# Optimization experiments

Measured on AMD Instinct MI355X. Metric: run time of the kernel, lower is better.

The kernel has to match this reference:

```python
import jax, jax.numpy as jnp
import numpy as np

NUM_HEADS = 12
LN_EPS = 1e-5
SM_EPS = 1e-6


def layer_norm(x, w, b):
    m = x.mean(-1, keepdims=True)
    v = ((x - m) ** 2).mean(-1, keepdims=True)
    return (x - m) / jnp.sqrt(v + LN_EPS) * w + b


def softmax_with_policy(attn, policy):
    # attn: [B,H,N,N], policy: [B,N,1]
    B, H, N, _ = attn.shape
    attn_policy = policy.reshape(B, 1, 1, N)
    eye = jnp.eye(N, dtype=attn.dtype)[None, None]
    attn_policy = attn_policy + (1.0 - attn_policy) * eye
    m = attn.max(axis=-1, keepdims=True)
    e = jnp.exp(attn - m) * attn_policy
    return (e + SM_EPS / N) / (e.sum(axis=-1, keepdims=True) + SM_EPS)


def create_ys(ncdf, n_ref):
    # ncdf: [B, N-1]; returns ys: [B, n_ref-1]
    B = ncdf.shape[0]
    ys = jnp.linspace(0.0, 1.0, n_ref - 1, dtype=ncdf.dtype)[None, :]
    ys_start = jnp.min(ncdf + (ncdf == 0).astype(ncdf.dtype) * 1e8, axis=1, keepdims=True)
    steps = jnp.arange(n_ref - 1, dtype=ncdf.dtype)[None, :]
    return ys_start + (ys * (n_ref - 2) - ys_start * steps) / (n_ref - 2)


def get_unique_indices(indices, max_value):
    # duplicate indices are replaced by max_value, then re-sorted
    B = indices.shape[0]
    s = jnp.sort(indices, axis=1)
    shifted = jnp.concatenate([s[:, 1:], jnp.ones((B, 1), s.dtype)], axis=1)
    uniq = jnp.where(shifted == s, max_value, s)
    return jnp.sort(uniq, axis=1)


def ats_block(x, policy, norm1_w, norm1_b, qkv_w, proj_w, proj_b,
              norm2_w, norm2_b, fc1_w, fc1_b, fc2_w, fc2_b,
              n_tokens, n_ref_tokens):
    B, N, C = x.shape
    H = NUM_HEADS
    dh = C // H
    scale = dh ** -0.5

    xn = layer_norm(x, norm1_w, norm1_b)
    qkv = (xn @ qkv_w).reshape(B, N, 3, H, dh).transpose(2, 0, 3, 1, 4)  # [3,B,H,N,dh]
    qkv = qkv * policy[None, :, None, :, :]
    q, k, v = qkv[0], qkv[1], qkv[2]

    attn = softmax_with_policy(jnp.einsum('bhnd,bhmd->bhnm', q, k) * scale, policy)

    # --- score assignment ---
    v_norm = jnp.linalg.norm(v.transpose(0, 2, 1, 3).reshape(B, N, C), axis=2)  # [B,N]
    sig = attn[:, :, 0, :].sum(axis=1) * v_norm      # CLS attention row summed over heads
    sig = sig[:, 1:]
    sig = sig / sig.sum(axis=1, keepdims=True)
    order = jnp.argsort(sig, axis=1)                 # ascending
    sorted_scores = jnp.take_along_axis(sig, order, axis=1)

    # --- inverse transform sampling ---
    cdf = jnp.cumsum(sorted_scores, axis=1)
    cmin = cdf.min(axis=1, keepdims=True)
    cmax = cdf.max(axis=1, keepdims=True)
    ncdf = (cdf - cmin) / (cmax - cmin)              # [B, N-1]
    ys = create_ys(ncdf, n_ref_tokens)               # [B, n_ref-1]
    diff = (n_ref_tokens - 1) - (N - 1)
    ncdf_p = jnp.pad(ncdf, ((0, 0), (diff, 0))) if diff > 0 else ncdf
    tokens_to_pick = jnp.argmin(jnp.abs(ys[:, :, None] - ncdf_p[:, None, :]), axis=2) - diff

    uniq = get_unique_indices(tokens_to_pick, N - 1)[:, :N - 1]
    ui = uniq[:, :n_tokens - 1]                      # [B, n_tokens-1]

    # reorder attn rows / raw tokens by significance order, pad a zero row at N-1
    oidx = jnp.broadcast_to(order[:, None, :, None], (B, H, N - 1, N))
    attn_sorted = jnp.take_along_axis(attn[:, :, 1:, :], oidx, axis=2)
    attn_tmp = jnp.pad(attn_sorted, ((0, 0), (0, 0), (0, 1), (0, 0)))
    rx_sorted = jnp.take_along_axis(x[:, 1:, :], jnp.broadcast_to(order[:, :, None], (B, N - 1, C)), axis=1)
    rx_tmp = jnp.pad(rx_sorted, ((0, 0), (0, 1), (0, 0)))

    uidx = jnp.broadcast_to(ui[:, None, :, None], (B, H, n_tokens - 1, N))
    attn_sel = jnp.take_along_axis(attn_tmp, uidx, axis=2)
    rx_sel = jnp.take_along_axis(rx_tmp, jnp.broadcast_to(ui[:, :, None], (B, n_tokens - 1, C)), axis=1)

    attn_new = jnp.concatenate([attn[:, :, 0:1, :], attn_sel], axis=2)     # [B,H,n_tokens,N]
    selected_x = jnp.concatenate([x[:, 0:1, :], rx_sel], axis=1)           # [B,n_tokens,C]
    pol_new = (ui != N - 1).astype(x.dtype)[:, :, None]
    pol_new = jnp.pad(pol_new, ((0, 0), (1, 0), (0, 0)), constant_values=1.0)  # [B,n_tokens,1]

    out = jnp.einsum('bhnm,bhmd->bhnd', attn_new, v)
    out = out.transpose(0, 2, 1, 3).reshape(B, n_tokens, C)
    out = (out @ proj_w + proj_b) * pol_new

    x2 = selected_x + out
    h = jax.nn.gelu(layer_norm(x2, norm2_w, norm2_b) @ fc1_w + fc1_b, approximate=False)
    x2 = x2 + (h @ fc2_w + fc2_b) * pol_new
    return x2, pol_new


def setup_inputs() -> dict:
    key = jax.random.key(0)
    ks = jax.random.split(key, 6)
    B, N, C = 8, 785, 768
    init = lambda k, sh, fan: jax.random.normal(k, sh, jnp.float32) * (fan ** -0.5)
    return {
        'x': jax.random.normal(ks[0], (B, N, C), jnp.float32),
        'policy': jnp.ones((B, N, 1), jnp.float32),
        'norm1_w': jnp.ones((C,), jnp.float32),
        'norm1_b': jnp.zeros((C,), jnp.float32),
        'qkv_w': init(ks[1], (C, 3 * C), C),
        'proj_w': init(ks[2], (C, C), C),
        'proj_b': jnp.zeros((C,), jnp.float32),
        'norm2_w': jnp.ones((C,), jnp.float32),
        'norm2_b': jnp.zeros((C,), jnp.float32),
        'fc1_w': init(ks[3], (C, 4 * C), C),
        'fc1_b': jnp.zeros((4 * C,), jnp.float32),
        'fc2_w': init(ks[4], (4 * C, C), 4 * C),
        'fc2_b': jnp.zeros((C,), jnp.float32),
        'n_tokens': 393,
        'n_ref_tokens': 785,
    }


def reference(x, policy, norm1_w, norm1_b, qkv_w, proj_w, proj_b,
              norm2_w, norm2_b, fc1_w, fc1_b, fc2_w, fc2_b,
              n_tokens, n_ref_tokens):
    return ats_block(x, policy, norm1_w, norm1_b, qkv_w, proj_w, proj_b,
                     norm2_w, norm2_b, fc1_w, fc1_b, fc2_w, fc2_b,
                     int(n_tokens), int(n_ref_tokens))
```

## Files before the change

kernel.cpp:

```cpp
#include <hip/hip_runtime.h>
#include <hip/hip_bf16.h>
#include <float.h>
#include <math.h>
#include <stdint.h>

constexpr int B_   = 8;
constexpr int N_   = 785;
constexpr int C_   = 768;
constexpr int H_   = 12;
constexpr int DH_  = 64;
constexpr int NT_  = 393;
constexpr int QKVC = 3 * C_;
constexpr int BN   = B_ * N_;
constexpr int BT   = B_ * NT_;
constexpr int MSEL = N_ - 1;
constexpr float  SCALE_F = 0.125f;
constexpr double LNEPS   = 1e-5;
constexpr double SMEPS   = 1e-6;

#define DEV static __device__ __forceinline__

typedef __hip_bfloat16 bf16;
typedef __attribute__((ext_vector_type(8))) short frag8;
typedef __attribute__((ext_vector_type(4))) float facc4;

DEV short f2b(float v) { return (short)__hip_bfloat16_raw(__float2bfloat16(v)).x; }
DEV float b2f(short s) {
  union { unsigned int u; float f; } cv;
  cv.u = ((unsigned int)(unsigned short)s) << 16;
  return cv.f;
}
DEV float gelu_exact(float v) { return 0.5f * v * (1.0f + erff(v * 0.70710678118654752f)); }

DEV double blockReduceSumD(double v, double* scratch, int nw) {
#pragma unroll
  for (int o = 32; o; o >>= 1) v += __shfl_xor(v, o);
  int lane = threadIdx.x & 63, wid = threadIdx.x >> 6;
  __syncthreads();
  if (lane == 0) scratch[wid] = v;
  __syncthreads();
  double r = scratch[0];
  for (int i = 1; i < nw; i++) r += scratch[i];
  return r;
}
DEV double blockReduceMaxD(double v, double* scratch, int nw) {
#pragma unroll
  for (int o = 32; o; o >>= 1) v = fmax(v, __shfl_xor(v, o));
  int lane = threadIdx.x & 63, wid = threadIdx.x >> 6;
  __syncthreads();
  if (lane == 0) scratch[wid] = v;
  __syncthreads();
  double r = scratch[0];
  for (int i = 1; i < nw; i++) r = fmax(r, scratch[i]);
  return r;
}
DEV float blockReduceSumF(float v, float* scratch, int nw) {
#pragma unroll
  for (int o = 32; o; o >>= 1) v += __shfl_xor(v, o);
  int lane = threadIdx.x & 63, wid = threadIdx.x >> 6;
  __syncthreads();
  if (lane == 0) scratch[wid] = v;
  __syncthreads();
  float r = scratch[0];
  for (int i = 1; i < nw; i++) r += scratch[i];
  return r;
}
DEV float blockReduceMaxF(float v, float* scratch, int nw) {
#pragma unroll
  for (int o = 32; o; o >>= 1) v = fmaxf(v, __shfl_xor(v, o));
  int lane = threadIdx.x & 63, wid = threadIdx.x >> 6;
  __syncthreads();
  if (lane == 0) scratch[wid] = v;
  __syncthreads();
  float r = scratch[0];
  for (int i = 1; i < nw; i++) r = fmaxf(r, scratch[i]);
  return r;
}

__global__ __launch_bounds__(256) void ln1_kernel(
    const float* __restrict__ x, const float* __restrict__ w, const float* __restrict__ b,
    double* __restrict__ xn64, bf16* __restrict__ xnb) {
  int row = blockIdx.x;
  int t = threadIdx.x;
  __shared__ double scr[8];
  const float* xr = x + (size_t)row * C_;
  double vals[3];
#pragma unroll
  for (int i = 0; i < 3; i++) vals[i] = (double)xr[t + i * 256];
  double s = vals[0] + vals[1] + vals[2];
  s = blockReduceSumD(s, scr, 4);
  double mean = s / (double)C_;
  double vs = 0.0;
#pragma unroll
  for (int i = 0; i < 3; i++) { double d = vals[i] - mean; vs += d * d; }
  vs = blockReduceSumD(vs, scr, 4);
  double inv = 1.0 / sqrt(vs / (double)C_ + LNEPS);
#pragma unroll
  for (int i = 0; i < 3; i++) {
    int c = t + i * 256;
    double o = (vals[i] - mean) * inv * (double)w[c] + (double)b[c];
    xn64[(size_t)row * C_ + c] = o;
    xnb[(size_t)row * C_ + c] = __float2bfloat16((float)o);
  }
}

__global__ __launch_bounds__(256) void transpose_bf16(
    const float* __restrict__ W, bf16* __restrict__ Wt, int K, int N) {
  __shared__ float tile[32][33];
  int k0 = blockIdx.y * 32, n0 = blockIdx.x * 32;
  int tx = threadIdx.x & 31, ty = threadIdx.x >> 5;
  for (int i = ty; i < 32; i += 8) {
    int k = k0 + i, n = n0 + tx;
    tile[i][tx] = (k < K && n < N) ? W[(size_t)k * N + n] : 0.f;
  }
  __syncthreads();
  for (int i = ty; i < 32; i += 8) {
    int n = n0 + i, k = k0 + tx;
    if (n < N && k < K) Wt[(size_t)n * K + k] = __float2bfloat16(tile[tx][i]);
  }
}

__global__ __launch_bounds__(256) void gemm128(
    const bf16* __restrict__ A, const bf16* __restrict__ Bt,
    float* __restrict__ Cc, const float* __restrict__ bias,
    const float* __restrict__ rowscale, int M, int K, int Ncols,
    bf16* __restrict__ gelu_bf) {
  __shared__ short As[128][40];
  __shared__ short Bs[128][40];
  const short* Ap = (const short*)A;
  const short* Bp = (const short*)Bt;
  int t = threadIdx.x;
  int n0 = blockIdx.x * 128;
  int m0 = blockIdx.y * 128;
  int w = t >> 6, l = t & 63;
  int wr = w >> 1, wc = w & 1;
  int srow = t >> 1;
  int koff = (t & 1) * 16;
  int fr = l & 15, fk = (l >> 4) * 8;
  facc4 acc[4][4] = {};
  for (int k0 = 0; k0 < K; k0 += 32) {
    int4 av0 = make_int4(0, 0, 0, 0), av1 = make_int4(0, 0, 0, 0);
    if (m0 + srow < M) {
      const short* ap = Ap + (size_t)(m0 + srow) * K + k0 + koff;
      av0 = *(const int4*)ap;
      av1 = *(const int4*)(ap + 8);
    }
    const short* bp = Bp + (size_t)(n0 + srow) * K + k0 + koff;
    int4 bv0 = *(const int4*)bp;
    int4 bv1 = *(const int4*)(bp + 8);
    *(int4*)(&As[srow][koff])     = av0;
    *(int4*)(&As[srow][koff + 8]) = av1;
    *(int4*)(&Bs[srow][koff])     = bv0;
    *(int4*)(&Bs[srow][koff + 8]) = bv1;
    __syncthreads();
    frag8 af[4], bf[4];
#pragma unroll
    for (int i = 0; i < 4; i++) af[i] = *(frag8*)(&As[wr * 64 + i * 16 + fr][fk]);
#pragma unroll
    for (int j = 0; j < 4; j++) bf[j] = *(frag8*)(&Bs[wc * 64 + j * 16 + fr][fk]);
#pragma unroll
    for (int i = 0; i < 4; i++)
#pragma unroll
      for (int j = 0; j < 4; j++)
        acc[i][j] = __builtin_amdgcn_mfma_f32_16x16x32_bf16(af[i], bf[j], acc[i][j], 0, 0, 0);
    __syncthreads();
  }
#pragma unroll
  for (int i = 0; i < 4; i++) {
#pragma unroll
    for (int reg = 0; reg < 4; reg++) {
      int row = m0 + wr * 64 + i * 16 + (l >> 4) * 4 + reg;
      if (row >= M) continue;
      float rs = rowscale ? rowscale[row] : 1.f;
#pragma unroll
      for (int j = 0; j < 4; j++) {
        int col = n0 + wc * 64 + j * 16 + fr;
        float v = acc[i][j][reg];
        if (bias) v += bias[col];
        if (gelu_bf) {
          gelu_bf[(size_t)row * Ncols + col] = __float2bfloat16(gelu_exact(v));
        } else {
          v *= rs;
          Cc[(size_t)row * Ncols + col] = v;
        }
      }
    }
  }
}

__global__ __launch_bounds__(256) void q0_kernel(
    const double* __restrict__ xn64, const float* __restrict__ qkvw,
    const float* __restrict__ policy, double* __restrict__ q064) {
  int b = blockIdx.x;
  int jc = blockIdx.y;
  int t = threadIdx.x;
  int jl = t & 63, ks = t >> 6;
  __shared__ double x0[C_];
  __shared__ double part[4][64];
  for (int i = t; i < C_; i += 256) x0[i] = xn64[(size_t)(b * N_) * C_ + i];
  __syncthreads();
  int j = jc * 64 + jl;
  const float* wp = qkvw + j;
  double a = 0.0;
  int c0 = ks * 192;
#pragma unroll 8
  for (int c = c0; c < c0 + 192; c++) a += x0[c] * (double)wp[(size_t)c * QKVC];
  part[ks][jl] = a;
  __syncthreads();
  if (t < 64) {
    double pol = (double)policy[b * N_];
    q064[b * C_ + jc * 64 + t] =
        (part[0][t] + part[1][t] + part[2][t] + part[3][t]) * pol;
  }
}

__global__ __launch_bounds__(256) void g_kernel(
    const double* __restrict__ q064, const float* __restrict__ qkvw,
    double* __restrict__ g64) {
  int bh = blockIdx.x;
  int b = bh / H_, h = bh % H_;
  int t = threadIdx.x;
  __shared__ double qh[DH_];
  if (t < DH_) qh[t] = q064[b * C_ + h * DH_ + t];
  __syncthreads();
  for (int c = t; c < C_; c += 256) {
    const float* wp = qkvw + (size_t)c * QKVC + C_ + h * DH_;
    double a = 0.0;
#pragma unroll 8
    for (int d = 0; d < DH_; d++) a += qh[d] * (double)wp[d];
    g64[(size_t)bh * C_ + c] = a;
  }
}

__global__ __launch_bounds__(256) void logits_kernel(
    const double* __restrict__ xn64, const double* __restrict__ g64,
    const float* __restrict__ policy, double* __restrict__ l64) {
  int row = blockIdx.x;
  int b = row / N_;
  int n = row % N_;
  int t = threadIdx.x;
  int w = t >> 6, lane = t & 63;
  __shared__ double xr[C_];
  for (int i = t; i < C_; i += 256) xr[i] = xn64[(size_t)row * C_ + i];
  __syncthreads();
  double pol = (double)policy[row];
#pragma unroll
  for (int hh = 0; hh < 3; hh++) {
    int h = w + hh * 4;
    const double* gp = g64 + (size_t)(b * H_ + h) * C_;
    double p = 0.0;
#pragma unroll 4
    for (int i = lane; i < C_; i += 64) p += xr[i] * gp[i];
#pragma unroll
    for (int o = 32; o; o >>= 1) p += __shfl_xor(p, o);
    if (lane == 0) l64[(size_t)(b * H_ + h) * N_ + n] = 0.125 * pol * p;
  }
}

__global__ __launch_bounds__(256) void vnorm_kernel(
    const double* __restrict__ xn64, const float* __restrict__ qkvw,
    const float* __restrict__ policy, double* __restrict__ vnorm2) {
  __shared__ double scr[8];
  int r0 = blockIdx.x * 8;
  int t = threadIdx.x;
  double acc[8][3] = {};
  const double* xb = xn64 + (size_t)r0 * C_;
  for (int c = 0; c < C_; c += 2) {
    const float* wp0 = qkvw + (size_t)c * QKVC + 2 * C_;
    const float* wp1 = wp0 + QKVC;
    double w00 = (double)wp0[t], w01 = (double)wp0[t + 256], w02 = (double)wp0[t + 512];
    double w10 = (double)wp1[t], w11 = (double)wp1[t + 256], w12 = (double)wp1[t + 512];
#pragma unroll
    for (int r = 0; r < 8; r++) {
      double x0 = xb[(size_t)r * C_ + c];
      double x1 = xb[(size_t)r * C_ + c + 1];
      acc[r][0] += x0 * w00; acc[r][1] += x0 * w01; acc[r][2] += x0 * w02;
      acc[r][0] += x1 * w10; acc[r][1] += x1 * w11; acc[r][2] += x1 * w12;
    }
  }
#pragma unroll
  for (int r = 0; r < 8; r++) {
    double p = acc[r][0] * acc[r][0] + acc[r][1] * acc[r][1] + acc[r][2] * acc[r][2];
    double s = blockReduceSumD(p, scr, 4);
    if (t == 0) {
      double pol = (double)policy[r0 + r];
      vnorm2[r0 + r] = s * pol * pol;
    }
  }
}

__global__ __launch_bounds__(256) void softmax0_kernel(
    double* __restrict__ l64, const float* __restrict__ policy) {
  int bh = blockIdx.x;
  int b = bh / H_;
  double* lp = l64 + (size_t)bh * N_;
  __shared__ double scr[8];
  int t = threadIdx.x;
  double mx = -1e300;
  for (int n = t; n < N_; n += 256) mx = fmax(mx, lp[n]);
  mx = blockReduceMaxD(mx, scr, 4);
  double ssum = 0.0;
  for (int n = t; n < N_; n += 256) {
    double pol = (double)policy[b * N_ + n];
    double w = (n == 0) ? 1.0 : pol;
    double e = exp(lp[n] - mx) * w;
    lp[n] = e;
    ssum += e;
  }
  ssum = blockReduceSumD(ssum, scr, 4);
  double denom = ssum + SMEPS;
  double addc = SMEPS / (double)N_;
  for (int n = t; n < N_; n += 256) lp[n] = (lp[n] + addc) / denom;
}

__global__ __launch_bounds__(1024) void select_kernel(
    const double* __restrict__ p0, const double* __restrict__ vnorm2,
    int* __restrict__ selidx, float* __restrict__ poln, float* __restrict__ out_pol) {
  int b = blockIdx.x;
  int t = threadIdx.x;
  __shared__ double sigv[MSEL];
  __shared__ double svals[MSEL];
  __shared__ double nc[MSEL];
  __shared__ int    ord[MSEL];
  __shared__ int    pick[MSEL];
  __shared__ int    spick[MSEL];
  __shared__ int    uq[MSEL];
  __shared__ int    suq[MSEL];
  __shared__ double sh_ys;

  if (t < MSEL) {
    int n = t + 1;
    double s = 0.0;
#pragma unroll
    for (int h = 0; h < H_; h++) s += p0[(size_t)(b * H_ + h) * N_ + n];
    sigv[t] = s * sqrt(vnorm2[b * N_ + n]);
  }
  __syncthreads();
  if (t < MSEL) {
    double v = sigv[t];
    int rank = 0;
    for (int i = 0; i < MSEL; i++) {
      double vi = sigv[i];
      rank += (vi < v) || (vi == v && i < t);
    }
    ord[rank] = t;
    svals[rank] = v;
  }
  __syncthreads();
  if (t == 0) {
    double a = 0.0;
    for (int i = 0; i < MSEL; i++) { a += svals[i]; svals[i] = a; }
  }
  __syncthreads();
  {
    double c0 = svals[0], cN = svals[MSEL - 1];
    if (t < MSEL) nc[t] = (svals[t] - c0) / (cN - c0);
  }
  __syncthreads();
  if (t == 0) {
    double m = 1e300;
    for (int i = 0; i < MSEL; i++) {
      double v = nc[i];
      if (v == 0.0) v += 100000000.0;
      m = fmin(m, v);
    }
    sh_ys = m;
  }
  __syncthreads();
  if (t < MSEL) {
    double s = sh_ys;
    double ysj = (t == MSEL - 1) ? 1.0 : (double)t / 783.0;
    double y = s + (ysj * 783.0 - s * (double)t) / 783.0;
    double bd = 1e300;
    int bi = 0;
    for (int i = 0; i < MSEL; i++) {
      double d = fabs(y - nc[i]);
      if (d < bd) { bd = d; bi = i; }
    }
    pick[t] = bi;
  }
  __syncthreads();
  if (t < MSEL) {
    int p = pick[t];
    int rank = 0;
    for (int i = 0; i < MSEL; i++) {
      int pi = pick[i];
      rank += (pi < p) || (pi == p && i < t);
    }
    spick[rank] = p;
  }
  __syncthreads();
  if (t < MSEL) {
    int s = spick[t];
    int nxt = (t < MSEL - 1) ? spick[t + 1] : 1;
    uq[t] = (nxt == s) ? MSEL : s;
  }
  __syncthreads();
  if (t < MSEL) {
    int u = uq[t];
    int rank = 0;
    for (int i = 0; i < MSEL; i++) {
      int ui = uq[i];
      rank += (ui < u) || (ui == u && i < t);
    }
    suq[rank] = u;
  }
  __syncthreads();
  if (t < NT_) {
    int sel, polI;
    if (t == 0) { sel = 0; polI = 1; }
    else {
      int ut = suq[t - 1];
      polI = (ut != MSEL) ? 1 : 0;
      sel = polI ? (ord[ut] + 1) : -1;
    }
    selidx[b * NT_ + t] = sel;
    poln[b * NT_ + t] = (float)polI;
    out_pol[b * NT_ + t] = (float)polI;
  }
}

__global__ __launch_bounds__(256) void flash_kernel(
    const float* __restrict__ qkv, const int* __restrict__ selidx,
    const float* __restrict__ policy, bf16* __restrict__ attn_bf) {
  int bh = blockIdx.y;
  int b = bh / H_, h = bh % H_;
  int j0 = blockIdx.x * 64;
  int t = threadIdx.x;
  int w = t >> 6, l = t & 63;
  __shared__ short Qs[64][72];
  __shared__ short Ks[64][72];
  __shared__ short Ps[64][72];
  __shared__ short Vs[64][72];
  __shared__ float pol_s[64];
  __shared__ float Vsum[64];

  {
    int jr = t >> 2, d0 = (t & 3) * 16;
    int j = j0 + jr;
    int r = (j < NT_) ? selidx[b * NT_ + j] : -1;
    if (r < 0) r = 0;
    const float* qp = qkv + (size_t)(b * N_ + r) * QKVC + h * DH_ + d0;
#pragma unroll
    for (int i = 0; i < 16; i++) Qs[jr][d0 + i] = f2b(qp[i]);
  }
  if (t < 64) Vsum[t] = 0.f;

  int frow = l & 15, fk = (l >> 4) * 8;
  int base_r = w * 16 + (l >> 4) * 4;
  int coln = l & 15;

  int rrow[4];
#pragma unroll
  for (int r = 0; r < 4; r++) {
    int j = j0 + base_r + r;
    rrow[r] = (j < NT_) ? selidx[b * NT_ + j] : -1;
  }
  float m_run[4] = {-1e30f, -1e30f, -1e30f, -1e30f};
  float s_run[4] = {0.f, 0.f, 0.f, 0.f};
  facc4 Oacc[4] = {{0, 0, 0, 0}, {0, 0, 0, 0}, {0, 0, 0, 0}, {0, 0, 0, 0}};

  for (int n0 = 0; n0 < 832; n0 += 64) {
    {
      int nr = t >> 2, d0 = (t & 3) * 16;
      int n = n0 + nr;
      bool ok = n < N_;
      const float* kp = qkv + (size_t)(b * N_ + (ok ? n : 0)) * QKVC + C_ + h * DH_ + d0;
#pragma unroll
      for (int i = 0; i < 16; i++) Ks[nr][d0 + i] = f2b(ok ? kp[i] : 0.f);
    }
    if (t < 64) {
      int n = n0 + t;
      pol_s[t] = (n < N_) ? policy[b * N_ + n] : 0.f;
    }
    __syncthreads();

    facc4 Sacc[4] = {{0, 0, 0, 0}, {0, 0, 0, 0}, {0, 0, 0, 0}, {0, 0, 0, 0}};
#pragma unroll
    for (int k0 = 0; k0 < 64; k0 += 32) {
      frag8 a = *(frag8*)(&Qs[w * 16 + frow][k0 + fk]);
#pragma unroll
      for (int nt = 0; nt < 4; nt++) {
        frag8 bb = *(frag8*)(&Ks[nt * 16 + frow][k0 + fk]);
        Sacc[nt] = __builtin_amdgcn_mfma_f32_16x16x32_bf16(a, bb, Sacc[nt], 0, 0, 0);
      }
    }
    float S[4][4];
    float tmax[4] = {-1e30f, -1e30f, -1e30f, -1e30f};
#pragma unroll
    for (int nt = 0; nt < 4; nt++) {
#pragma unroll
      for (int r = 0; r < 4; r++) {
        int n = n0 + nt * 16 + coln;
        float v = (n < N_) ? Sacc[nt][r] * SCALE_F : -1e30f;
        S[nt][r] = v;
        tmax[r] = fmaxf(tmax[r], v);
      }
    }
#pragma unroll
    for (int o = 1; o < 16; o <<= 1) {
#pragma unroll
      for (int r = 0; r < 4; r++) tmax[r] = fmaxf(tmax[r], __shfl_xor(tmax[r], o));
    }
    float m_new[4], scl[4], psum[4];
#pragma unroll
    for (int r = 0; r < 4; r++) {
      m_new[r] = fmaxf(m_run[r], tmax[r]);
      scl[r] = expf(m_run[r] - m_new[r]);
      psum[r] = 0.f;
    }
#pragma unroll
    for (int nt = 0; nt < 4; nt++) {
      float pol = pol_s[nt * 16 + coln];
      int n = n0 + nt * 16 + coln;
#pragma unroll
      for (int r = 0; r < 4; r++) {
        float wgt = (n == rrow[r]) ? 1.f : pol;
        float e = expf(S[nt][r] - m_new[r]) * wgt;
        S[nt][r] = e;
        psum[r] += e;
      }
    }
#pragma unroll
    for (int o = 1; o < 16; o <<= 1) {
#pragma unroll
      for (int r = 0; r < 4; r++) psum[r] += __shfl_xor(psum[r], o);
    }
#pragma unroll
    for (int r = 0; r < 4; r++) {
      s_run[r] = s_run[r] * scl[r] + psum[r];
      m_run[r] = m_new[r];
    }
    __syncthreads();

#pragma unroll
    for (int nt = 0; nt < 4; nt++) {
#pragma unroll
      for (int r = 0; r < 4; r++) Ps[base_r + r][nt * 16 + coln] = f2b(S[nt][r]);
    }
    {
      int nr = t >> 2, d0 = (t & 3) * 16;
      int n = n0 + nr;
      bool ok = n < N_;
      const float* vp = qkv + (size_t)(b * N_ + (ok ? n : 0)) * QKVC + 2 * C_ + h * DH_ + d0;
#pragma unroll
      for (int i = 0; i < 16; i++) Vs[d0 + i][nr] = f2b(ok ? vp[i] : 0.f);
    }
    __syncthreads();

    if (t < 64) {
      float a = 0.f;
#pragma unroll 16
      for (int k = 0; k < 64; k++) a += b2f(Vs[t][k]);
      Vsum[t] += a;
    }
#pragma unroll
    for (int dt = 0; dt < 4; dt++) {
#pragma unroll
      for (int r = 0; r < 4; r++) Oacc[dt][r] *= scl[r];
    }
#pragma unroll
    for (int k0 = 0; k0 < 64; k0 += 32) {
      frag8 a = *(frag8*)(&Ps[w * 16 + frow][k0 + fk]);
#pragma unroll
      for (int dt = 0; dt < 4; dt++) {
        frag8 bb = *(frag8*)(&Vs[dt * 16 + frow][k0 + fk]);
        Oacc[dt] = __builtin_amdgcn_mfma_f32_16x16x32_bf16(a, bb, Oacc[dt], 0, 0, 0);
      }
    }
  }
  __syncthreads();
  float addc = 1e-6f / (float)N_;
#pragma unroll
  for (int r = 0; r < 4; r++) {
    int j = j0 + base_r + r;
    if (j >= NT_) continue;
    float denom = s_run[r] + 1e-6f;
#pragma unroll
    for (int dt = 0; dt < 4; dt++) {
      int d = dt * 16 + coln;
      float val = (Oacc[dt][r] + addc * Vsum[d]) / denom;
      attn_bf[(size_t)(b * NT_ + j) * C_ + h * DH_ + d] = __float2bfloat16(val);
    }
  }
}

__global__ __launch_bounds__(256) void e2_kernel(
    const float* __restrict__ cbuf, const float* __restrict__ poln,
    const int* __restrict__ selidx, const float* __restrict__ x, float* __restrict__ x2) {
  int row = blockIdx.x;
  int t = threadIdx.x;
  int b = row / NT_;
  int r = selidx[row];
  float pn = poln[row];
  for (int i = t; i < C_; i += 256) {
    float sx = (r >= 0) ? x[(size_t)(b * N_ + r) * C_ + i] : 0.f;
    x2[(size_t)row * C_ + i] = sx + cbuf[(size_t)row * C_ + i] * pn;
  }
}

__global__ __launch_bounds__(256) void ln2_kernel(
    const float* __restrict__ xin, const float* __restrict__ w, const float* __restrict__ b,
    bf16* __restrict__ xoutb) {
  int row = blockIdx.x;
  int t = threadIdx.x;
  __shared__ float scr[8];
  const float* xr = xin + (size_t)row * C_;
  float vals[3];
#pragma unroll
  for (int i = 0; i < 3; i++) vals[i] = xr[t + i * 256];
  float s = vals[0] + vals[1] + vals[2];
  s = blockReduceSumF(s, scr, 4);
  float mean = s / (float)C_;
  float vs = 0.f;
#pragma unroll
  for (int i = 0; i < 3; i++) { float d = vals[i] - mean; vs += d * d; }
  vs = blockReduceSumF(vs, scr, 4);
  float sd = sqrtf(vs / (float)C_ + 1e-5f);
#pragma unroll
  for (int i = 0; i < 3; i++) {
    int c = t + i * 256;
    xoutb[(size_t)row * C_ + c] =
        __float2bfloat16((vals[i] - mean) / sd * w[c] + b[c]);
  }
}

__global__ __launch_bounds__(256) void e4_kernel(
    const float* __restrict__ x2, const float* __restrict__ cbuf,
    const float* __restrict__ poln, float* __restrict__ out) {
  int row = blockIdx.x;
  int t = threadIdx.x;
  float pn = poln[row];
  for (int i = t; i < C_; i += 256) {
    float v = x2[(size_t)row * C_ + i] + cbuf[(size_t)row * C_ + i] * pn;
    out[(size_t)row * C_ + i] = v;
  }
}

extern "C" void kernel_launch(void* const* d_in, const int* in_sizes, int n_in,
                              void* d_out, int out_size, void* d_ws, size_t ws_size,
                              hipStream_t stream) {
  const float* x      = (const float*)d_in[0];
  const float* policy = (const float*)d_in[1];
  const float* n1w    = (const float*)d_in[2];
  const float* n1b    = (const float*)d_in[3];
  const float* qkvw   = (const float*)d_in[4];
  const float* projw  = (const float*)d_in[5];
  const float* projb  = (const float*)d_in[6];
  const float* n2w    = (const float*)d_in[7];
  const float* n2b    = (const float*)d_in[8];
  const float* fc1w   = (const float*)d_in[9];
  const float* fc1b   = (const float*)d_in[10];
  const float* fc2w   = (const float*)d_in[11];
  const float* fc2b   = (const float*)d_in[12];

  char* ws = (char*)d_ws;
  size_t off = 0;
  auto alloc = [&](size_t bytes) {
    size_t o = off;
    off += (bytes + 255) & ~(size_t)255;
    return o;
  };

  double* xn64    = (double*)(ws + alloc((size_t)BN * C_ * 8));
  bf16*   xnb     = (bf16*)(ws + alloc((size_t)BN * C_ * 2));
  float*  qkv32   = (float*)(ws + alloc((size_t)BN * QKVC * 4));
  double* vnorm2  = (double*)(ws + alloc((size_t)BN * 8));
  double* q064    = (double*)(ws + alloc((size_t)B_ * C_ * 8));
  double* g64     = (double*)(ws + alloc((size_t)B_ * H_ * C_ * 8));
  double* l64     = (double*)(ws + alloc((size_t)B_ * H_ * N_ * 8));
  int*    selidx  = (int*)(ws + alloc((size_t)BT * 4));
  float*  poln    = (float*)(ws + alloc((size_t)BT * 4));
  bf16*   attn_bf = (bf16*)(ws + alloc((size_t)BT * C_ * 2));
  float*  cbuf    = (float*)(ws + alloc((size_t)BT * C_ * 4));
  float*  x2      = (float*)(ws + alloc((size_t)BT * C_ * 4));
  bf16*   qkvw_t  = (bf16*)(ws + alloc((size_t)QKVC * C_ * 2));
  bf16*   projw_t = (bf16*)(ws + alloc((size_t)C_ * C_ * 2));
  bf16*   fc1w_t  = (bf16*)(ws + alloc((size_t)4 * C_ * C_ * 2));
  bf16*   fc2w_t  = (bf16*)(ws + alloc((size_t)C_ * 4 * C_ * 2));
  bf16*   xn2b    = (bf16*)(ws + alloc((size_t)BT * C_ * 2));
  bf16*   h_bf    = (bf16*)(ws + alloc((size_t)BT * 4 * C_ * 2));
  if (off > ws_size) return;

  float* out_x = (float*)d_out;
  float* out_p = out_x + (size_t)BT * C_;

  transpose_bf16<<<dim3(QKVC / 32, C_ / 32), 256, 0, stream>>>(qkvw, qkvw_t, C_, QKVC);
  transpose_bf16<<<dim3(C_ / 32, C_ / 32), 256, 0, stream>>>(projw, projw_t, C_, C_);
  transpose_bf16<<<dim3(4 * C_ / 32, C_ / 32), 256, 0, stream>>>(fc1w, fc1w_t, C_, 4 * C_);
  transpose_bf16<<<dim3(C_ / 32, 4 * C_ / 32), 256, 0, stream>>>(fc2w, fc2w_t, 4 * C_, C_);

  ln1_kernel<<<BN, 256, 0, stream>>>(x, n1w, n1b, xn64, xnb);

  {
    dim3 g(QKVC / 128, (BN + 127) / 128);
    gemm128<<<g, 256, 0, stream>>>(xnb, qkvw_t, qkv32, nullptr, policy, BN, C_, QKVC, nullptr);
  }

  q0_kernel<<<dim3(B_, C_ / 64), 256, 0, stream>>>(xn64, qkvw, policy, q064);
  g_kernel<<<B_ * H_, 256, 0, stream>>>(q064, qkvw, g64);
  logits_kernel<<<BN, 256, 0, stream>>>(xn64, g64, policy, l64);
  vnorm_kernel<<<BN / 8, 256, 0, stream>>>(xn64, qkvw, policy, vnorm2);
  softmax0_kernel<<<B_ * H_, 256, 0, stream>>>(l64, policy);
  select_kernel<<<B_, 1024, 0, stream>>>(l64, vnorm2, selidx, poln, out_p);

  {
    dim3 g((NT_ + 63) / 64, B_ * H_);
    flash_kernel<<<g, 256, 0, stream>>>(qkv32, selidx, policy, attn_bf);
  }

  {
    dim3 g(C_ / 128, (BT + 127) / 128);
    gemm128<<<g, 256, 0, stream>>>(attn_bf, projw_t, cbuf, projb, nullptr, BT, C_, C_, nullptr);
  }
  e2_kernel<<<BT, 256, 0, stream>>>(cbuf, poln, selidx, x, x2);
  ln2_kernel<<<BT, 256, 0, stream>>>(x2, n2w, n2b, xn2b);
  {
    dim3 g(4 * C_ / 128, (BT + 127) / 128);
    gemm128<<<g, 256, 0, stream>>>(xn2b, fc1w_t, nullptr, fc1b, nullptr, BT, C_, 4 * C_, h_bf);
  }
  {
    dim3 g(C_ / 128, (BT + 127) / 128);
    gemm128<<<g, 256, 0, stream>>>(h_bf, fc2w_t, cbuf, fc2b, nullptr, BT, 4 * C_, C_, nullptr);
  }
  e4_kernel<<<BT, 256, 0, stream>>>(x2, cbuf, poln, out_x);
}
```

Measured before the change: 923.5 us.

## Fuse residual epilogues into proj and fc2 GEMMs with 64x64 tiles

Adds a 64x64-tile bf16 MFMA GEMM whose epilogue applies the residual gather from x scaled by poln (proj) or the x2 residual (fc2). The separate e2 and e4 elementwise kernels and the cbuf intermediate go away. The smaller tiles also give more blocks for the N=768 GEMMs (12x50 instead of 6x25), which should fill more of the CUs. The trade-off is less data reuse per tile and a single-buffered loop with one MFMA column-strip per wave, and the fused epilogue does scattered residual reads.

```diff
diff --git a/kernel.cpp b/kernel.cpp
--- a/kernel.cpp
+++ b/kernel.cpp
@@ -117,6 +117,70 @@
   for (int i = ty; i < 32; i += 8) {
     int n = n0 + i, k = k0 + tx;
     if (n < N && k < K) Wt[(size_t)n * K + k] = __float2bfloat16(tile[tx][i]);
+  }
+}
+
+__global__ __launch_bounds__(256) void gemm_bf16(
+    const bf16* __restrict__ A, const bf16* __restrict__ Bt,
+    float* __restrict__ Cc, const float* __restrict__ bias,
+    const float* __restrict__ rowscale, int M, int K, int Ncols,
+    int mode, const float* __restrict__ xg, const int* __restrict__ selidx_,
+    const float* __restrict__ poln_, const float* __restrict__ res) {
+  __shared__ short As[64][40];
+  __shared__ short Bs[64][40];
+  const short* Ap = (const short*)A;
+  const short* Bp = (const short*)Bt;
+  int t = threadIdx.x;
+  int n0 = blockIdx.x * 64;
+  int m0 = blockIdx.y * 64;
+  int w = t >> 6, l = t & 63;
+  int srow = t >> 2;
+  int koff = (t & 3) * 8;
+  facc4 acc[4] = {{0, 0, 0, 0}, {0, 0, 0, 0}, {0, 0, 0, 0}, {0, 0, 0, 0}};
+  int frow = (l & 15);
+  int fk = (l >> 4) * 8;
+  for (int k0 = 0; k0 < K; k0 += 32) {
+    {
+      int4 av = make_int4(0, 0, 0, 0);
+      if (m0 + srow < M)
+        av = *(const int4*)(Ap + (size_t)(m0 + srow) * K + k0 + koff);
+      *(int4*)(&As[srow][koff]) = av;
+      int4 bv = *(const int4*)(Bp + (size_t)(n0 + srow) * K + k0 + koff);
+      *(int4*)(&Bs[srow][koff]) = bv;
+    }
+    __syncthreads();
+    frag8 a = *(frag8*)(&As[w * 16 + frow][fk]);
+#pragma unroll
+    for (int nt = 0; nt < 4; nt++) {
+      frag8 bfr = *(frag8*)(&Bs[nt * 16 + frow][fk]);
+      acc[nt] = __builtin_amdgcn_mfma_f32_16x16x32_bf16(a, bfr, acc[nt], 0, 0, 0);
+    }
+    __syncthreads();
+  }
+#pragma unroll
+  for (int reg = 0; reg < 4; reg++) {
+    int row = m0 + w * 16 + (l >> 4) * 4 + reg;
+    if (row >= M) continue;
+    float rs = (mode == 0 && rowscale) ? rowscale[row] : 1.f;
+    float pn = (mode != 0) ? poln_[row] : 0.f;
+    int rsel = (mode == 1) ? selidx_[row] : 0;
+    int bI = (mode == 1) ? (row / NT_) : 0;
+#pragma unroll
+    for (int nt = 0; nt < 4; nt++) {
+      int col = n0 + nt * 16 + (l & 15);
+      float v = acc[nt][reg];
+      if (bias) v += bias[col];
+      float outv;
+      if (mode == 0) {
+        outv = v * rs;
+      } else if (mode == 1) {
+        float sx = (rsel >= 0) ? xg[(size_t)(bI * N_ + rsel) * C_ + col] : 0.f;
+        outv = sx + v * pn;
+      } else {
+        outv = res[(size_t)row * Ncols + col] + v * pn;
+      }
+      Cc[(size_t)row * Ncols + col] = outv;
+    }
   }
 }
 
@@ -585,20 +649,6 @@
   }
 }
 
-__global__ __launch_bounds__(256) void e2_kernel(
-    const float* __restrict__ cbuf, const float* __restrict__ poln,
-    const int* __restrict__ selidx, const float* __restrict__ x, float* __restrict__ x2) {
-  int row = blockIdx.x;
-  int t = threadIdx.x;
-  int b = row / NT_;
-  int r = selidx[row];
-  float pn = poln[row];
-  for (int i = t; i < C_; i += 256) {
-    float sx = (r >= 0) ? x[(size_t)(b * N_ + r) * C_ + i] : 0.f;
-    x2[(size_t)row * C_ + i] = sx + cbuf[(size_t)row * C_ + i] * pn;
-  }
-}
-
 __global__ __launch_bounds__(256) void ln2_kernel(
     const float* __restrict__ xin, const float* __restrict__ w, const float* __restrict__ b,
     bf16* __restrict__ xoutb) {
@@ -622,18 +672,6 @@
     int c = t + i * 256;
     xoutb[(size_t)row * C_ + c] =
         __float2bfloat16((vals[i] - mean) / sd * w[c] + b[c]);
-  }
-}
-
-__global__ __launch_bounds__(256) void e4_kernel(
-    const float* __restrict__ x2, const float* __restrict__ cbuf,
-    const float* __restrict__ poln, float* __restrict__ out) {
-  int row = blockIdx.x;
-  int t = threadIdx.x;
-  float pn = poln[row];
-  for (int i = t; i < C_; i += 256) {
-    float v = x2[(size_t)row * C_ + i] + cbuf[(size_t)row * C_ + i] * pn;
-    out[(size_t)row * C_ + i] = v;
   }
 }
 
@@ -672,7 +710,6 @@
   int*    selidx  = (int*)(ws + alloc((size_t)BT * 4));
   float*  poln    = (float*)(ws + alloc((size_t)BT * 4));
   bf16*   attn_bf = (bf16*)(ws + alloc((size_t)BT * C_ * 2));
-  float*  cbuf    = (float*)(ws + alloc((size_t)BT * C_ * 4));
   float*  x2      = (float*)(ws + alloc((size_t)BT * C_ * 4));
   bf16*   qkvw_t  = (bf16*)(ws + alloc((size_t)QKVC * C_ * 2));
   bf16*   projw_t = (bf16*)(ws + alloc((size_t)C_ * C_ * 2));
@@ -710,18 +747,18 @@
   }
 
   {
-    dim3 g(C_ / 128, (BT + 127) / 128);
-    gemm128<<<g, 256, 0, stream>>>(attn_bf, projw_t, cbuf, projb, nullptr, BT, C_, C_, nullptr);
-  }
-  e2_kernel<<<BT, 256, 0, stream>>>(cbuf, poln, selidx, x, x2);
+    dim3 g(C_ / 64, (BT + 63) / 64);
+    gemm_bf16<<<g, 256, 0, stream>>>(attn_bf, projw_t, x2, projb, nullptr, BT, C_, C_,
+                                     1, x, selidx, poln, nullptr);
+  }
   ln2_kernel<<<BT, 256, 0, stream>>>(x2, n2w, n2b, xn2b);
   {
     dim3 g(4 * C_ / 128, (BT + 127) / 128);
     gemm128<<<g, 256, 0, stream>>>(xn2b, fc1w_t, nullptr, fc1b, nullptr, BT, C_, 4 * C_, h_bf);
   }
   {
-    dim3 g(C_ / 128, (BT + 127) / 128);
-    gemm128<<<g, 256, 0, stream>>>(h_bf, fc2w_t, cbuf, fc2b, nullptr, BT, 4 * C_, C_, nullptr);
-  }
-  e4_kernel<<<BT, 256, 0, stream>>>(x2, cbuf, poln, out_x);
-}
+    dim3 g(C_ / 64, (BT + 63) / 64);
+    gemm_bf16<<<g, 256, 0, stream>>>(h_bf, fc2w_t, out_x, fc2b, nullptr, BT, 4 * C_, C_,
+                                     2, nullptr, nullptr, poln, x2);
+  }
+}
```

New measurement: 886.7 us. -4.0%, faster.
